# Kernel optimization log

Measured on AMD Instinct MI355X. Metric: run time of the kernel, lower is better.

The kernel has to match this reference:

```python
import jax, jax.numpy as jnp
import numpy as np

PS = 7          # window_size
HEADS = 8
DIM = 64
EPS = 1e-12     # F.normalize default eps


def resize_bilinear(x, oh, ow, align_corners):
    """PyTorch-style bilinear resize for NCHW tensors (antialias=False)."""
    b, c, h, w = x.shape
    if align_corners:
        ys = jnp.linspace(0.0, h - 1.0, oh, dtype=x.dtype)
        xs = jnp.linspace(0.0, w - 1.0, ow, dtype=x.dtype)
    else:
        ys = jnp.maximum((jnp.arange(oh, dtype=x.dtype) + 0.5) * (h / oh) - 0.5, 0.0)
        xs = jnp.maximum((jnp.arange(ow, dtype=x.dtype) + 0.5) * (w / ow) - 0.5, 0.0)
    y0 = jnp.floor(ys).astype(jnp.int32)
    x0 = jnp.floor(xs).astype(jnp.int32)
    y1 = jnp.minimum(y0 + 1, h - 1)
    x1 = jnp.minimum(x0 + 1, w - 1)
    ly = (ys - y0.astype(x.dtype))[None, None, :, None]   # (1,1,oh,1)
    lx = (xs - x0.astype(x.dtype))[None, None, None, :]   # (1,1,1,ow)
    rows = x[:, :, y0, :] * (1.0 - ly) + x[:, :, y1, :] * ly       # (b,c,oh,w)
    out = rows[:, :, :, x0] * (1.0 - lx) + rows[:, :, :, x1] * lx  # (b,c,oh,ow)
    return out


def _to_windows(t, b, heads, d, ps, xb, yb):
    # 'b (head d) (x h ph) (y w pw) -> (b x y) head d (w ph) (pw h)'
    t = t.reshape(b, heads, d, xb, ps, ps, yb, ps, ps)  # b,head,d,x,h,ph,y,w,pw
    t = t.transpose(0, 3, 6, 1, 2, 7, 5, 8, 4)          # b,x,y,head,d,w,ph,pw,h
    return t.reshape(b * xb * yb, heads, d, ps * ps, ps * ps)


def _from_windows(t, b, heads, d, ps, xb, yb):
    # inverse rearrange back to (b, head*d, x*ps*ps, y*ps*ps)
    t = t.reshape(b, xb, yb, heads, d, ps, ps, ps, ps)  # b,x,y,head,d,w,ph,pw,h
    t = t.transpose(0, 3, 4, 1, 8, 6, 2, 5, 7)          # b,head,d,x,h,ph,y,w,pw
    return t.reshape(b, heads * d, xb * ps * ps, yb * ps * ps)


def setup_inputs() -> dict:
    key = jax.random.key(0)
    k1, k2, k3, k4 = jax.random.split(key, 4)
    x = jax.random.normal(k1, (4, DIM, 256, 256), jnp.float32)
    qkv_w = jax.random.normal(k2, (3 * DIM, DIM), jnp.float32) * 0.05
    dw_w = jax.random.normal(k3, (3 * DIM, 1, 3, 3), jnp.float32) * 0.05
    proj_w = jax.random.normal(k4, (DIM, DIM), jnp.float32) * 0.05
    return {"x": x, "qkv_w": qkv_w, "dw_w": dw_w, "proj_w": proj_w}


def reference(x, qkv_w, dw_w, proj_w):
    b, c, h, w = x.shape
    heads, ps = HEADS, PS
    ps2 = ps * ps
    temph = -(-h // ps2) * ps2   # next multiple of ps^2 (matches while loop)
    tempw = -(-w // ps2) * ps2
    d = c // heads

    # conv1x1 (qkv) then depthwise 3x3 conv
    qkv = jnp.einsum('bchw,oc->bohw', x, qkv_w)
    qkv = jax.lax.conv_general_dilated(
        qkv, dw_w, window_strides=(1, 1), padding=((1, 1), (1, 1)),
        feature_group_count=3 * c,
        dimension_numbers=('NCHW', 'OIHW', 'NCHW'))

    # pad by bilinear interpolation, align_corners=True
    qkv = resize_bilinear(qkv, temph, tempw, align_corners=True)
    q, k, v = jnp.split(qkv, 3, axis=1)

    xb, yb = temph // ps2, tempw // ps2
    q = _to_windows(q, b, heads, d, ps, xb, yb)  # (b*xb*yb, heads, d, 49, 49)
    k = _to_windows(k, b, heads, d, ps, xb, yb)
    v = _to_windows(v, b, heads, d, ps, xb, yb)

    # L2-normalized (cosine) attention along the last axis, no temperature
    qn = q / jnp.maximum(jnp.linalg.norm(q, axis=-1, keepdims=True), EPS)
    kn = k / jnp.maximum(jnp.linalg.norm(k, axis=-1, keepdims=True), EPS)
    attn = jax.nn.softmax(qn @ jnp.swapaxes(kn, -1, -2), axis=-1)
    out = attn @ v

    out = _from_windows(out, b, heads, d, ps, xb, yb)
    out = resize_bilinear(out, h, w, align_corners=False)
    return jnp.einsum('bchw,oc->bohw', out, proj_w)
```

## Files before the change

### kernel.cpp

```cpp
#include <hip/hip_runtime.h>
#include <math.h>

#define BATCH 4
#define CIN 64
#define HW 256
#define NPIX 65536
#define OC 192
#define TH 294
#define NPIX_R 86436
#define PS2 49
#define NWIN 36
#define WCPB 2304
#define KSTR 52

__device__ __forceinline__ float rl_f32(float v, int lane) {
    return __uint_as_float(__builtin_amdgcn_readlane(__float_as_uint(v), lane));
}

__global__ __launch_bounds__(256)
void k_qkv1x1(const float* __restrict__ x, const float* __restrict__ w,
              float* __restrict__ A) {
    __shared__ float wT[64][64];
    __shared__ float xs[64][256];
    x += (size_t)blockIdx.z * CIN * NPIX;
    A += (size_t)blockIdx.z * OC * NPIX;
    const int tid = threadIdx.x;
    const int pxbase = blockIdx.x * 256;
    const int ocbase = blockIdx.y * 64;

    for (int idx = tid; idx < 1024; idx += 256) {
        int o = idx >> 4, c4 = idx & 15;
        float4 v = *reinterpret_cast<const float4*>(w + (size_t)(ocbase + o) * CIN + c4 * 4);
        wT[c4 * 4 + 0][o] = v.x; wT[c4 * 4 + 1][o] = v.y;
        wT[c4 * 4 + 2][o] = v.z; wT[c4 * 4 + 3][o] = v.w;
    }
    for (int idx = tid; idx < 4096; idx += 256) {
        int c = idx >> 6, p4 = idx & 63;
        float4 v = *reinterpret_cast<const float4*>(x + (size_t)c * NPIX + pxbase + p4 * 4);
        *reinterpret_cast<float4*>(&xs[c][p4 * 4]) = v;
    }
    __syncthreads();

    const int tx = tid & 15, ty = tid >> 4;
    float acc[4][16];
    #pragma unroll
    for (int a = 0; a < 4; ++a)
        #pragma unroll
        for (int b = 0; b < 16; ++b) acc[a][b] = 0.f;

    #pragma unroll 4
    for (int k = 0; k < 64; ++k) {
        float4 wv = *reinterpret_cast<const float4*>(&wT[k][ty * 4]);
        float wr[4] = {wv.x, wv.y, wv.z, wv.w};
        float xv[16];
        #pragma unroll
        for (int i = 0; i < 4; ++i) {
            float4 v = *reinterpret_cast<const float4*>(&xs[k][tx * 4 + i * 64]);
            xv[i * 4 + 0] = v.x; xv[i * 4 + 1] = v.y;
            xv[i * 4 + 2] = v.z; xv[i * 4 + 3] = v.w;
        }
        #pragma unroll
        for (int a = 0; a < 4; ++a)
            #pragma unroll
            for (int b = 0; b < 16; ++b)
                acc[a][b] = fmaf(wr[a], xv[b], acc[a][b]);
    }

    #pragma unroll
    for (int a = 0; a < 4; ++a) {
        float* Ap = A + (size_t)(ocbase + ty * 4 + a) * NPIX + pxbase;
        #pragma unroll
        for (int i = 0; i < 4; ++i)
            *reinterpret_cast<float4*>(Ap + tx * 4 + i * 64) =
                make_float4(acc[a][i * 4 + 0], acc[a][i * 4 + 1],
                            acc[a][i * 4 + 2], acc[a][i * 4 + 3]);
    }
}

__global__ __launch_bounds__(256)
void k_dw3x3(const float* __restrict__ A, const float* __restrict__ dwv,
             float* __restrict__ Bf) {
    A  += (size_t)blockIdx.z * OC * NPIX;
    Bf += (size_t)blockIdx.z * OC * NPIX;
    int gid = blockIdx.x * 256 + threadIdx.x;
    int ch = gid >> 14;
    int q  = gid & 16383;
    int y  = q >> 6;
    int x4 = (q & 63) << 2;
    const float* Ap = A + (size_t)ch * NPIX;
    float wv[9];
    #pragma unroll
    for (int i = 0; i < 9; ++i) wv[i] = dwv[ch * 9 + i];
    float acc0 = 0.f, acc1 = 0.f, acc2 = 0.f, acc3 = 0.f;
    #pragma unroll
    for (int ky = 0; ky < 3; ++ky) {
        int yy = y + ky - 1;
        if (yy < 0 || yy >= HW) continue;
        const float* row = Ap + yy * HW;
        float cv[6];
        #pragma unroll
        for (int t = 0; t < 6; ++t) {
            int xx = x4 - 1 + t;
            cv[t] = (xx >= 0 && xx < HW) ? row[xx] : 0.f;
        }
        #pragma unroll
        for (int kx = 0; kx < 3; ++kx) {
            float wk = wv[ky * 3 + kx];
            acc0 = fmaf(cv[0 + kx], wk, acc0);
            acc1 = fmaf(cv[1 + kx], wk, acc1);
            acc2 = fmaf(cv[2 + kx], wk, acc2);
            acc3 = fmaf(cv[3 + kx], wk, acc3);
        }
    }
    *reinterpret_cast<float4*>(Bf + (size_t)ch * NPIX + y * HW + x4) =
        make_float4(acc0, acc1, acc2, acc3);
}

#define PIN4(v) asm volatile("" : "+v"(v.x), "+v"(v.y), "+v"(v.z), "+v"(v.w))
#define SQ4(v) fmaf(v.x, v.x, fmaf(v.y, v.y, fmaf(v.z, v.z, v.w * v.w)))
#define DOT4(KV, OFS) { float4 q_ = *reinterpret_cast<const float4*>(qr + (OFS)); \
    dd0 = fmaf(q_.x, KV.x, dd0); dd1 = fmaf(q_.y, KV.y, dd1); \
    dd2 = fmaf(q_.z, KV.z, dd2); dd3 = fmaf(q_.w, KV.w, dd3); }
#define PV4(VV, J) { \
    o0 = fmaf(rl_f32(p, (J)+0), VV.x, o0); o1 = fmaf(rl_f32(p, (J)+1), VV.y, o1); \
    o2 = fmaf(rl_f32(p, (J)+2), VV.z, o2); o3 = fmaf(rl_f32(p, (J)+3), VV.w, o3); }
#define VC(jj) (act ? Vs[(jj) * KSTR + l] : 1.0f)

__global__ __launch_bounds__(256, 4)
void k_attn(const float* __restrict__ Bf, float* __restrict__ Cf) {
    __shared__ float Qs[PS2 * KSTR];
    __shared__ float Ks[PS2 * KSTR];
    __shared__ float Vs[PS2 * KSTR];
    Bf += (size_t)blockIdx.z * OC * NPIX;
    Cf += (size_t)blockIdx.z * (size_t)CIN * NPIX_R;
    const int tid = threadIdx.x;
    const int wv = tid >> 6, lane = tid & 63;
    const int wc  = blockIdx.x;
    const int ch  = wc & 63;
    const int win = wc >> 6;
    const int xw  = win / 6, yw = win - xw * 6;
    const float* qb = Bf + (size_t)ch * NPIX;
    const float* kb = qb + (size_t)64  * NPIX;
    const float* vb = qb + (size_t)128 * NPIX;
    const float scale = 255.0f / 293.0f;

    for (int e = tid; e < PS2 * PS2; e += 256) {
        int rl = e / PS2;
        int cl = e - rl * PS2;
        int gy = xw * PS2 + rl, gx = yw * PS2 + cl;
        float sy = gy * scale, sx = gx * scale;
        int y0 = (int)sy, x0 = (int)sx;
        float ly = sy - y0, lx = sx - x0;
        int y1 = min(y0 + 1, HW - 1), x1 = min(x0 + 1, HW - 1);
        float w00 = (1.f - ly) * (1.f - lx), w01 = (1.f - ly) * lx;
        float w10 = ly * (1.f - lx),         w11 = ly * lx;
        int o00 = y0 * HW + x0, o01 = y0 * HW + x1;
        int o10 = y1 * HW + x0, o11 = y1 * HW + x1;
        int i = (cl / 7) * 7 + (rl % 7);
        int j = (cl % 7) * 7 + (rl / 7);
        int d = i * KSTR + j;
        Qs[d] = qb[o00] * w00 + qb[o01] * w01 + qb[o10] * w10 + qb[o11] * w11;
        Ks[d] = kb[o00] * w00 + kb[o01] * w01 + kb[o10] * w10 + kb[o11] * w11;
        Vs[d] = vb[o00] * w00 + vb[o01] * w01 + vb[o10] * w10 + vb[o11] * w11;
    }
    __syncthreads();

    const int l = min(lane, PS2 - 1);
    const bool act = (lane < PS2);

    const float* kr0 = &Ks[l * KSTR];
    float4 k0  = *reinterpret_cast<const float4*>(kr0 + 0);
    float4 k1  = *reinterpret_cast<const float4*>(kr0 + 4);
    float4 k2  = *reinterpret_cast<const float4*>(kr0 + 8);
    float4 k3  = *reinterpret_cast<const float4*>(kr0 + 12);
    float4 k4  = *reinterpret_cast<const float4*>(kr0 + 16);
    float4 k5  = *reinterpret_cast<const float4*>(kr0 + 20);
    float4 k6  = *reinterpret_cast<const float4*>(kr0 + 24);
    float4 k7  = *reinterpret_cast<const float4*>(kr0 + 28);
    float4 k8  = *reinterpret_cast<const float4*>(kr0 + 32);
    float4 k9  = *reinterpret_cast<const float4*>(kr0 + 36);
    float4 k10 = *reinterpret_cast<const float4*>(kr0 + 40);
    float4 k11 = *reinterpret_cast<const float4*>(kr0 + 44);
    float  k48 = kr0[48];
    PIN4(k0); PIN4(k1); PIN4(k2); PIN4(k3); PIN4(k4); PIN4(k5);
    PIN4(k6); PIN4(k7); PIN4(k8); PIN4(k9); PIN4(k10); PIN4(k11);

    float kss = SQ4(k0) + SQ4(k1) + SQ4(k2) + SQ4(k3) + SQ4(k4) + SQ4(k5)
              + SQ4(k6) + SQ4(k7) + SQ4(k8) + SQ4(k9) + SQ4(k10) + SQ4(k11)
              + k48 * k48;
    const float inkl = 1.f / fmaxf(sqrtf(kss), 1e-12f);

    float4 v0  = make_float4(VC(0),  VC(1),  VC(2),  VC(3));
    float4 v1  = make_float4(VC(4),  VC(5),  VC(6),  VC(7));
    float4 v2  = make_float4(VC(8),  VC(9),  VC(10), VC(11));
    float4 v3  = make_float4(VC(12), VC(13), VC(14), VC(15));
    float4 v4  = make_float4(VC(16), VC(17), VC(18), VC(19));
    float4 v5  = make_float4(VC(20), VC(21), VC(22), VC(23));
    float4 v6  = make_float4(VC(24), VC(25), VC(26), VC(27));
    float4 v7  = make_float4(VC(28), VC(29), VC(30), VC(31));
    float4 v8  = make_float4(VC(32), VC(33), VC(34), VC(35));
    float4 v9  = make_float4(VC(36), VC(37), VC(38), VC(39));
    float4 v10 = make_float4(VC(40), VC(41), VC(42), VC(43));
    float4 v11 = make_float4(VC(44), VC(45), VC(46), VC(47));
    float  v48 = VC(48);
    PIN4(v0); PIN4(v1); PIN4(v2); PIN4(v3); PIN4(v4); PIN4(v5);
    PIN4(v6); PIN4(v7); PIN4(v8); PIN4(v9); PIN4(v10); PIN4(v11);
    asm volatile("" : "+v"(k48), "+v"(v48));

    float inql;
    {
        const float* qrl = &Qs[l * KSTR];
        float qss = 0.f;
        #pragma unroll
        for (int u = 0; u < 12; ++u) {
            float4 t = *reinterpret_cast<const float4*>(qrl + u * 4);
            qss += SQ4(t);
        }
        float q48 = qrl[48];
        qss = fmaf(q48, q48, qss);
        inql = 1.f / fmaxf(sqrtf(qss), 1e-12f);
    }
    __syncthreads();

    for (int i = wv; i < PS2; i += 4) {
        const float inq_i = rl_f32(inql, i);
        const float* qr = &Qs[i * KSTR];
        float dd0 = 0.f, dd1 = 0.f, dd2 = 0.f, dd3 = 0.f;
        DOT4(k0, 0)   DOT4(k1, 4)   DOT4(k2, 8)   DOT4(k3, 12)
        DOT4(k4, 16)  DOT4(k5, 20)  DOT4(k6, 24)  DOT4(k7, 28)
        DOT4(k8, 32)  DOT4(k9, 36)  DOT4(k10, 40) DOT4(k11, 44)
        float dsum = (dd0 + dd1) + (dd2 + dd3);
        dsum = fmaf(qr[48], k48, dsum);
        float p = __expf(dsum * inkl * inq_i);

        float o0 = 0.f, o1 = 0.f, o2 = 0.f, o3 = 0.f;
        PV4(v0, 0)   PV4(v1, 4)   PV4(v2, 8)   PV4(v3, 12)
        PV4(v4, 16)  PV4(v5, 20)  PV4(v6, 24)  PV4(v7, 28)
        PV4(v8, 32)  PV4(v9, 36)  PV4(v10, 40) PV4(v11, 44)
        float ot = (o0 + o1) + (o2 + o3);
        ot = fmaf(rl_f32(p, 48), v48, ot);
        float ssum = rl_f32(ot, 49);
        float res = ot * __builtin_amdgcn_rcpf(ssum);
        if (act) Qs[i * KSTR + lane] = res;
    }
    __syncthreads();

    float* cb = Cf + (size_t)ch * NPIX_R;
    for (int e = tid; e < PS2 * PS2; e += 256) {
        int rl = e / PS2;
        int cl = e - rl * PS2;
        int i = (cl / 7) * 7 + (rl % 7);
        int j = (cl % 7) * 7 + (rl / 7);
        cb[(xw * PS2 + rl) * TH + (yw * PS2 + cl)] = Qs[i * KSTR + j];
    }
}

__global__ __launch_bounds__(256)
void k_down(const float* __restrict__ Cf, float* __restrict__ D) {
    Cf += (size_t)blockIdx.z * (size_t)CIN * NPIX_R;
    D  += (size_t)blockIdx.z * (size_t)CIN * NPIX;
    int gid = blockIdx.x * 256 + threadIdx.x;
    int ch = gid >> 14;
    int q  = gid & 16383;
    int y  = q >> 6;
    int x4 = (q & 63) << 2;
    const float sc = 294.0f / 256.0f;
    float sy = fmaxf((y + 0.5f) * sc - 0.5f, 0.f);
    int y0 = (int)sy;
    float ly = sy - y0;
    int y1 = min(y0 + 1, TH - 1);
    const float* r0 = Cf + (size_t)ch * NPIX_R + y0 * TH;
    const float* r1 = Cf + (size_t)ch * NPIX_R + y1 * TH;
    float res[4];
    #pragma unroll
    for (int t = 0; t < 4; ++t) {
        float sx = fmaxf((x4 + t + 0.5f) * sc - 0.5f, 0.f);
        int x0 = (int)sx;
        float lx = sx - x0;
        int x1 = min(x0 + 1, TH - 1);
        res[t] = (r0[x0] * (1.f - lx) + r0[x1] * lx) * (1.f - ly)
               + (r1[x0] * (1.f - lx) + r1[x1] * lx) * ly;
    }
    *reinterpret_cast<float4*>(D + (size_t)ch * NPIX + y * HW + x4) =
        make_float4(res[0], res[1], res[2], res[3]);
}

__global__ __launch_bounds__(256)
void k_pmm(const float* __restrict__ D, const float* __restrict__ w,
           float* __restrict__ out) {
    __shared__ float wT[64][64];
    __shared__ float xs[64][256];
    D   += (size_t)blockIdx.z * CIN * NPIX;
    out += (size_t)blockIdx.z * CIN * NPIX;
    const int tid = threadIdx.x;
    const int pxbase = blockIdx.x * 256;

    for (int idx = tid; idx < 1024; idx += 256) {
        int o = idx >> 4, c4 = idx & 15;
        float4 v = *reinterpret_cast<const float4*>(w + (size_t)o * CIN + c4 * 4);
        wT[c4 * 4 + 0][o] = v.x; wT[c4 * 4 + 1][o] = v.y;
        wT[c4 * 4 + 2][o] = v.z; wT[c4 * 4 + 3][o] = v.w;
    }
    for (int idx = tid; idx < 4096; idx += 256) {
        int c = idx >> 6, p4 = idx & 63;
        float4 v = *reinterpret_cast<const float4*>(D + (size_t)c * NPIX + pxbase + p4 * 4);
        *reinterpret_cast<float4*>(&xs[c][p4 * 4]) = v;
    }
    __syncthreads();

    const int tx = tid & 15, ty = tid >> 4;
    float acc[4][16];
    #pragma unroll
    for (int a = 0; a < 4; ++a)
        #pragma unroll
        for (int b = 0; b < 16; ++b) acc[a][b] = 0.f;

    #pragma unroll 4
    for (int k = 0; k < 64; ++k) {
        float4 wv = *reinterpret_cast<const float4*>(&wT[k][ty * 4]);
        float wr[4] = {wv.x, wv.y, wv.z, wv.w};
        float xv[16];
        #pragma unroll
        for (int i = 0; i < 4; ++i) {
            float4 v = *reinterpret_cast<const float4*>(&xs[k][tx * 4 + i * 64]);
            xv[i * 4 + 0] = v.x; xv[i * 4 + 1] = v.y;
            xv[i * 4 + 2] = v.z; xv[i * 4 + 3] = v.w;
        }
        #pragma unroll
        for (int a = 0; a < 4; ++a)
            #pragma unroll
            for (int b = 0; b < 16; ++b)
                acc[a][b] = fmaf(wr[a], xv[b], acc[a][b]);
    }

    #pragma unroll
    for (int a = 0; a < 4; ++a) {
        float* op = out + (size_t)(ty * 4 + a) * NPIX + pxbase;
        #pragma unroll
        for (int i = 0; i < 4; ++i)
            *reinterpret_cast<float4*>(op + tx * 4 + i * 64) =
                make_float4(acc[a][i * 4 + 0], acc[a][i * 4 + 1],
                            acc[a][i * 4 + 2], acc[a][i * 4 + 3]);
    }
}

extern "C" void kernel_launch(void* const* d_in, const int* in_sizes, int n_in,
                              void* d_out, int out_size, void* d_ws, size_t ws_size,
                              hipStream_t stream) {
    const float* x   = (const float*)d_in[0];
    const float* qw  = (const float*)d_in[1];
    const float* dwv = (const float*)d_in[2];
    const float* pw  = (const float*)d_in[3];
    float* out = (float*)d_out;

    const size_t perAB = (size_t)OC * NPIX;
    const size_t needBig = (size_t)2 * BATCH * perAB * sizeof(float);
    const size_t needMid = (size_t)2 * 2 * perAB * sizeof(float);

    int NB;
    if (ws_size >= needBig)      NB = BATCH;
    else if (ws_size >= needMid) NB = 2;
    else                         NB = 1;

    float* A = (float*)d_ws;
    float* B = A + (size_t)NB * perAB;
    float* C = A;
    float* D = A + (size_t)NB * CIN * NPIX_R;

    for (int b = 0; b < BATCH; b += NB) {
        const float* xb = x + (size_t)b * CIN * NPIX;
        float* ob = out + (size_t)b * CIN * NPIX;
        hipLaunchKernelGGL(k_qkv1x1, dim3(256, 3, NB),   dim3(256), 0, stream, xb, qw, A);
        hipLaunchKernelGGL(k_dw3x3,  dim3(12288, 1, NB), dim3(256), 0, stream, A, dwv, B);
        hipLaunchKernelGGL(k_attn,   dim3(WCPB, 1, NB),  dim3(256), 0, stream, B, C);
        hipLaunchKernelGGL(k_down,   dim3(4096, 1, NB),  dim3(256), 0, stream, C, D);
        hipLaunchKernelGGL(k_pmm,    dim3(256, 1, NB),   dim3(256), 0, stream, D, pw, ob);
    }
}
```

Baseline: 553.7 us.

## Precompute bilinear gather tables, widen depthwise conv to 8 pixels per thread

Adds a small prep kernel that precomputes, for each window, the bilinear source offsets and weights plus the window permutation and output offset tables. The attention kernel reads these tables instead of recomputing divisions and modulos per element. The depthwise 3x3 conv now handles 8 pixels per thread with float4 loads, and the attention launch-bounds occupancy hint drops from 4 to 2. The tables add extra global reads and a launch, and the T region placement within the workspace depends on ws_size.

```diff
diff --git a/kernel.cpp b/kernel.cpp
--- a/kernel.cpp
+++ b/kernel.cpp
@@ -9,9 +9,11 @@
 #define TH 294
 #define NPIX_R 86436
 #define PS2 49
+#define C2N 2401
 #define NWIN 36
 #define WCPB 2304
 #define KSTR 52
+#define TABN (NWIN * C2N)
 
 __device__ __forceinline__ float rl_f32(float v, int lane) {
     return __uint_as_float(__builtin_amdgcn_readlane(__float_as_uint(v), lane));
@@ -83,37 +85,64 @@
     A  += (size_t)blockIdx.z * OC * NPIX;
     Bf += (size_t)blockIdx.z * OC * NPIX;
     int gid = blockIdx.x * 256 + threadIdx.x;
-    int ch = gid >> 14;
-    int q  = gid & 16383;
-    int y  = q >> 6;
-    int x4 = (q & 63) << 2;
+    int ch = gid >> 13;
+    int q  = gid & 8191;
+    int y  = q >> 5;
+    int x8 = (q & 31) << 3;
     const float* Ap = A + (size_t)ch * NPIX;
     float wv[9];
     #pragma unroll
     for (int i = 0; i < 9; ++i) wv[i] = dwv[ch * 9 + i];
-    float acc0 = 0.f, acc1 = 0.f, acc2 = 0.f, acc3 = 0.f;
+    float a[8];
+    #pragma unroll
+    for (int t = 0; t < 8; ++t) a[t] = 0.f;
     #pragma unroll
     for (int ky = 0; ky < 3; ++ky) {
         int yy = y + ky - 1;
         if (yy < 0 || yy >= HW) continue;
         const float* row = Ap + yy * HW;
-        float cv[6];
-        #pragma unroll
-        for (int t = 0; t < 6; ++t) {
-            int xx = x4 - 1 + t;
-            cv[t] = (xx >= 0 && xx < HW) ? row[xx] : 0.f;
-        }
+        float4 m0 = *reinterpret_cast<const float4*>(row + x8);
+        float4 m1 = *reinterpret_cast<const float4*>(row + x8 + 4);
+        float lm = (x8 > 0)       ? row[x8 - 1] : 0.f;
+        float rp = (x8 < HW - 8)  ? row[x8 + 8] : 0.f;
+        float cv[10] = {lm, m0.x, m0.y, m0.z, m0.w, m1.x, m1.y, m1.z, m1.w, rp};
         #pragma unroll
         for (int kx = 0; kx < 3; ++kx) {
             float wk = wv[ky * 3 + kx];
-            acc0 = fmaf(cv[0 + kx], wk, acc0);
-            acc1 = fmaf(cv[1 + kx], wk, acc1);
-            acc2 = fmaf(cv[2 + kx], wk, acc2);
-            acc3 = fmaf(cv[3 + kx], wk, acc3);
+            #pragma unroll
+            for (int t = 0; t < 8; ++t)
+                a[t] = fmaf(cv[t + kx], wk, a[t]);
         }
     }
-    *reinterpret_cast<float4*>(Bf + (size_t)ch * NPIX + y * HW + x4) =
-        make_float4(acc0, acc1, acc2, acc3);
+    float* op = Bf + (size_t)ch * NPIX + y * HW + x8;
+    *reinterpret_cast<float4*>(op)     = make_float4(a[0], a[1], a[2], a[3]);
+    *reinterpret_cast<float4*>(op + 4) = make_float4(a[4], a[5], a[6], a[7]);
+}
+
+__global__ __launch_bounds__(256)
+void k_prep(int4* __restrict__ itab, float4* __restrict__ wtab,
+            int* __restrict__ dtab, int* __restrict__ otab) {
+    const int w = blockIdx.x;
+    const int xw = w / 6, yw = w - xw * 6;
+    const float scale = 255.0f / 293.0f;
+    for (int e = threadIdx.x; e < C2N; e += 256) {
+        int rl = e / PS2, cl = e - rl * PS2;
+        float sy = (float)(xw * PS2 + rl) * scale;
+        float sx = (float)(yw * PS2 + cl) * scale;
+        int y0 = (int)sy, x0 = (int)sx;
+        float ly = sy - y0, lx = sx - x0;
+        int y1 = min(y0 + 1, HW - 1), x1 = min(x0 + 1, HW - 1);
+        itab[w * C2N + e] = make_int4(y0 * HW + x0, y0 * HW + x1,
+                                      y1 * HW + x0, y1 * HW + x1);
+        wtab[w * C2N + e] = make_float4((1.f - ly) * (1.f - lx), (1.f - ly) * lx,
+                                        ly * (1.f - lx),         ly * lx);
+        if (w == 0) {
+            int i = (cl / 7) * 7 + rl % 7;
+            int j = (cl % 7) * 7 + rl / 7;
+            dtab[e] = i * KSTR + j;
+            otab[e] = rl * TH + cl;
+        }
+    }
 }
 
 #define PIN4(v) asm volatile("" : "+v"(v.x), "+v"(v.y), "+v"(v.z), "+v"(v.w))
@@ -126,8 +155,11 @@
     o2 = fmaf(rl_f32(p, (J)+2), VV.z, o2); o3 = fmaf(rl_f32(p, (J)+3), VV.w, o3); }
 #define VC(jj) (act ? Vs[(jj) * KSTR + l] : 1.0f)
 
-__global__ __launch_bounds__(256, 4)
-void k_attn(const float* __restrict__ Bf, float* __restrict__ Cf) {
+__global__ __launch_bounds__(256, 2)
+void k_attn(const float* __restrict__ Bf,
+            const int4* __restrict__ itab, const float4* __restrict__ wtab,
+            const int* __restrict__ dtab, const int* __restrict__ otab,
+            float* __restrict__ Cf) {
     __shared__ float Qs[PS2 * KSTR];
     __shared__ float Ks[PS2 * KSTR];
     __shared__ float Vs[PS2 * KSTR];
@@ -142,26 +174,15 @@
     const float* qb = Bf + (size_t)ch * NPIX;
     const float* kb = qb + (size_t)64  * NPIX;
     const float* vb = qb + (size_t)128 * NPIX;
-    const float scale = 255.0f / 293.0f;
-
-    for (int e = tid; e < PS2 * PS2; e += 256) {
-        int rl = e / PS2;
-        int cl = e - rl * PS2;
-        int gy = xw * PS2 + rl, gx = yw * PS2 + cl;
-        float sy = gy * scale, sx = gx * scale;
-        int y0 = (int)sy, x0 = (int)sx;
-        float ly = sy - y0, lx = sx - x0;
-        int y1 = min(y0 + 1, HW - 1), x1 = min(x0 + 1, HW - 1);
-        float w00 = (1.f - ly) * (1.f - lx), w01 = (1.f - ly) * lx;
-        float w10 = ly * (1.f - lx),         w11 = ly * lx;
-        int o00 = y0 * HW + x0, o01 = y0 * HW + x1;
-        int o10 = y1 * HW + x0, o11 = y1 * HW + x1;
-        int i = (cl / 7) * 7 + (rl % 7);
-        int j = (cl % 7) * 7 + (rl / 7);
-        int d = i * KSTR + j;
-        Qs[d] = qb[o00] * w00 + qb[o01] * w01 + qb[o10] * w10 + qb[o11] * w11;
-        Ks[d] = kb[o00] * w00 + kb[o01] * w01 + kb[o10] * w10 + kb[o11] * w11;
-        Vs[d] = vb[o00] * w00 + vb[o01] * w01 + vb[o10] * w10 + vb[o11] * w11;
+    const int wbase = win * C2N;
+
+    for (int e = tid; e < C2N; e += 256) {
+        int4   o  = itab[wbase + e];
+        float4 wt = wtab[wbase + e];
+        int    d  = dtab[e];
+        Qs[d] = qb[o.x] * wt.x + qb[o.y] * wt.y + qb[o.z] * wt.z + qb[o.w] * wt.w;
+        Ks[d] = kb[o.x] * wt.x + kb[o.y] * wt.y + kb[o.z] * wt.z + kb[o.w] * wt.w;
+        Vs[d] = vb[o.x] * wt.x + vb[o.y] * wt.y + vb[o.z] * wt.z + vb[o.w] * wt.w;
     }
     __syncthreads();
 
@@ -245,14 +266,9 @@
     }
     __syncthreads();
 
-    float* cb = Cf + (size_t)ch * NPIX_R;
-    for (int e = tid; e < PS2 * PS2; e += 256) {
-        int rl = e / PS2;
-        int cl = e - rl * PS2;
-        int i = (cl / 7) * 7 + (rl % 7);
-        int j = (cl % 7) * 7 + (rl / 7);
-        cb[(xw * PS2 + rl) * TH + (yw * PS2 + cl)] = Qs[i * KSTR + j];
-    }
+    float* cb = Cf + (size_t)ch * NPIX_R + (xw * PS2) * TH + yw * PS2;
+    for (int e = tid; e < C2N; e += 256)
+        cb[otab[e]] = Qs[dtab[e]];
 }
 
 __global__ __launch_bounds__(256)
@@ -366,14 +382,22 @@
     float* B = A + (size_t)NB * perAB;
     float* C = A;
     float* D = A + (size_t)NB * CIN * NPIX_R;
+    float* T = A + (size_t)NB * (CIN * NPIX_R + CIN * NPIX);
+    int4*   itab = (int4*)T;
+    float4* wtab = (float4*)(T + (size_t)TABN * 4);
+    int*    dtab = (int*)(T + (size_t)TABN * 8);
+    int*    otab = dtab + C2N;
 
     for (int b = 0; b < BATCH; b += NB) {
         const float* xb = x + (size_t)b * CIN * NPIX;
         float* ob = out + (size_t)b * CIN * NPIX;
-        hipLaunchKernelGGL(k_qkv1x1, dim3(256, 3, NB),   dim3(256), 0, stream, xb, qw, A);
-        hipLaunchKernelGGL(k_dw3x3,  dim3(12288, 1, NB), dim3(256), 0, stream, A, dwv, B);
-        hipLaunchKernelGGL(k_attn,   dim3(WCPB, 1, NB),  dim3(256), 0, stream, B, C);
-        hipLaunchKernelGGL(k_down,   dim3(4096, 1, NB),  dim3(256), 0, stream, C, D);
-        hipLaunchKernelGGL(k_pmm,    dim3(256, 1, NB),   dim3(256), 0, stream, D, pw, ob);
-    }
-}
+        hipLaunchKernelGGL(k_qkv1x1, dim3(256, 3, NB),  dim3(256), 0, stream, xb, qw, A);
+        hipLaunchKernelGGL(k_dw3x3,  dim3(6144, 1, NB), dim3(256), 0, stream, A, dwv, B);
+        hipLaunchKernelGGL(k_prep,   dim3(NWIN, 1, 1),  dim3(256), 0, stream,
+                           itab, wtab, dtab, otab);
+        hipLaunchKernelGGL(k_attn,   dim3(WCPB, 1, NB), dim3(256), 0, stream,
+                           B, itab, wtab, dtab, otab, C);
+        hipLaunchKernelGGL(k_down,   dim3(4096, 1, NB), dim3(256), 0, stream, C, D);
+        hipLaunchKernelGGL(k_pmm,    dim3(256, 1, NB),  dim3(256), 0, stream, D, pw, ob);
+    }
+}
```

New measurement: 558.3 us. About the same (+0.8%).
